# Kernel optimization log

Hardware: AMD Instinct MI355X
Metric: run time of the kernel (lower is better)

## Reference

```python
import jax, jax.numpy as jnp
import numpy as np
from jax import lax

EPS = 1e-12

def _l2norm(v, axis):
    n = jnp.linalg.norm(v, axis=axis, keepdims=True)
    return v / jnp.maximum(n, EPS)

def setup_inputs() -> dict:
    key = jax.random.key(0)
    k1, k2, k3 = jax.random.split(key, 3)
    C, H, W, K = 512, 192, 192, 64
    x = jax.random.normal(k1, (C, H, W), dtype=jnp.float32)
    conv_w = jax.random.normal(k2, (K, C), dtype=jnp.float32) * 0.05  # 1x1 conv, no bias (vladv2=False)
    centroids = jax.random.uniform(k3, (K, C), dtype=jnp.float32)
    return {"x": x, "conv_w": conv_w, "centroids": centroids}

def reference(x, conv_w, centroids):
    K = conv_w.shape[0]
    x4 = x[None]                      # [1,C,H,W]
    N, C, H, W = x4.shape
    L = H * W
    # descriptor-wise L2 normalization over channels
    x4 = _l2norm(x4, axis=1)
    # 1x1 conv -> soft assignment over clusters
    logits = jnp.einsum('kc,nchw->nkhw', conv_w, x4)
    soft = jax.nn.softmax(logits, axis=1)          # [N,K,H,W]
    sa_flat = soft.reshape(N, K, L)
    # top-2 cluster indices per location (argmax + second largest)
    _, top2 = lax.top_k(sa_flat.transpose(0, 2, 1), 2)  # [N,L,2]
    first, second = top2[..., 0], top2[..., 1]
    # unfold 3x3, padding 1: windows [N, L, K, 9] in (kh,kw) order
    pad = jnp.pad(soft, ((0, 0), (0, 0), (1, 1), (1, 1)))
    patches = jnp.stack([pad[:, :, di:di + H, dj:dj + W]
                         for di in range(3) for dj in range(3)], axis=2)  # [N,K,9,H,W]
    windows = patches.reshape(N, K, 9, L).transpose(0, 3, 1, 2)           # [N,L,K,9]
    # keep only windows of the top-2 clusters at each location
    karange = jnp.arange(K)[None, None, :]
    keep = (karange == first[:, :, None]) | (karange == second[:, :, None])  # [N,L,K]
    wsel = windows * keep[..., None].astype(windows.dtype)
    # fold (transpose of unfold): overlap-add back to [N,K,H,W]
    ws = wsel.transpose(0, 2, 3, 1).reshape(N, K, 9, H, W)
    out_pad = jnp.zeros((N, K, H + 2, W + 2), dtype=ws.dtype)
    t = 0
    for di in range(3):
        for dj in range(3):
            out_pad = out_pad.at[:, :, di:di + H, dj:dj + W].add(ws[:, :, t])
            t += 1
    weight = out_pad[:, :, 1:H + 1, 1:W + 1]
    # border mask: (min distance to border)^4
    ii = jnp.arange(H); jj = jnp.arange(W)
    mi = jnp.minimum(H - 1 - ii, ii)[:, None]
    mj = jnp.minimum(W - 1 - jj, jj)[None, :]
    m = jnp.minimum(mi, mj).astype(weight.dtype)
    m2 = m * m
    mask = m2 * m2
    weight = weight * mask[None, None]
    sa2 = weight.reshape(N, K, L)
    # per-cluster residual accumulation, vectorized (replaces the 64-iter loop)
    xf = x4.reshape(N, C, L)
    vlad = jnp.einsum('nkl,ncl->nkc', sa2, xf) - sa2.sum(-1)[..., None] * centroids[None]
    vlad = _l2norm(vlad, axis=2)               # intra-normalization
    v = vlad.reshape(N, -1)
    v = _l2norm(v, axis=1)
    return v
```

## Files before the change

kernel.cpp:

```cpp
#include <hip/hip_runtime.h>

#define HH 192
#define WW 192
#define LL (HH * WW)
#define CC 512
#define KK 64
#define EPSF 1e-12f
typedef unsigned long long ull;
typedef unsigned int uint;
typedef unsigned short ushort;

#define NCHUNK 192
#define CHUNKL (LL / NCHUNK)

typedef short bf16x8 __attribute__((ext_vector_type(8)));
typedef float f32x4 __attribute__((ext_vector_type(4)));

__device__ inline void split3(float v, ushort& h, ushort& md, ushort& lo) {
    uint b  = __float_as_uint(v);
    uint hb = b & 0xFFFF0000u;
    float r1 = v - __uint_as_float(hb);
    uint mb = __float_as_uint(r1) & 0xFFFF0000u;
    float r2 = r1 - __uint_as_float(mb);
    uint lb = __float_as_uint(r2) & 0xFFFF0000u;
    h = (ushort)(hb >> 16); md = (ushort)(mb >> 16); lo = (ushort)(lb >> 16);
}

__device__ inline void split2(float v, ushort& h, ushort& lo) {
    uint b  = __float_as_uint(v);
    uint hb = b & 0xFFFF0000u;
    float r = v - __uint_as_float(hb);
    h = (ushort)(hb >> 16); lo = (ushort)(__float_as_uint(r) >> 16);
}

__global__ __launch_bounds__(256) void k0_prep(const float* __restrict__ w,
                                               ushort* __restrict__ Whi,
                                               ushort* __restrict__ Wmid,
                                               ushort* __restrict__ Wlo,
                                               float* __restrict__ Szero) {
    int idx = blockIdx.x * 256 + threadIdx.x;
    int k = idx >> 9;
    int c = idx & 511;
    int s = c >> 5, w32 = c & 31, quad = w32 >> 3, j = w32 & 7;
    int kg = k >> 4, m = k & 15;
    int dst = (((s * 4 + kg) * 4 + quad) * 16 + m) * 8 + j;
    float v = w[idx];
    ushort h, md, lo;
    split3(v, h, md, lo);
    Whi[dst] = h; Wmid[dst] = md; Wlo[dst] = lo;
    if (blockIdx.x == 0 && threadIdx.x < 128) Szero[threadIdx.x] = 0.f;
}

__global__ __launch_bounds__(256) void k1_logits(const float* __restrict__ x,
                                                 const ushort* __restrict__ Whi,
                                                 const ushort* __restrict__ Wmid,
                                                 const ushort* __restrict__ Wlo,
                                                 float* __restrict__ soft,
                                                 float* __restrict__ invn,
                                                 ull* __restrict__ keep) {
    __shared__ float accL[3][32][64];
    __shared__ float ssL[3][2][64];
    int t = threadIdx.x, lane = t & 63, wid = t >> 6;
    int m = lane & 15, quad = lane >> 4;
    int pb = blockIdx.x * 32;
    int s16base = wid * 4;

    f32x4 acc[4][2];
#pragma unroll
    for (int kg = 0; kg < 4; ++kg)
#pragma unroll
        for (int cg = 0; cg < 2; ++cg) acc[kg][cg] = (f32x4){0.f, 0.f, 0.f, 0.f};
    float ssA[2] = {0.f, 0.f};

    const float* xq = x + (size_t)(wid * 128 + quad * 8) * LL + pb + m;

    bf16x8 Ah[2][4], Am[2][4], Al[2][4];
    float xv[2][2][8];

#pragma unroll
    for (int kg = 0; kg < 4; ++kg) {
        size_t off = (size_t)(((s16base * 4 + kg) * 64 + lane) * 8);
        Ah[0][kg] = *(const bf16x8*)(Whi  + off);
        Am[0][kg] = *(const bf16x8*)(Wmid + off);
        Al[0][kg] = *(const bf16x8*)(Wlo  + off);
    }
#pragma unroll
    for (int j = 0; j < 8; ++j) {
        const float* xr = xq + (size_t)j * LL;
        xv[0][0][j] = xr[0];
        xv[0][1][j] = xr[16];
    }

#pragma unroll
    for (int s = 0; s < 4; ++s) {
        const int cur = s & 1, nxt = cur ^ 1;
        if (s < 3) {
            int s16 = s16base + s + 1;
#pragma unroll
            for (int kg = 0; kg < 4; ++kg) {
                size_t off = (size_t)(((s16 * 4 + kg) * 64 + lane) * 8);
                Ah[nxt][kg] = *(const bf16x8*)(Whi  + off);
                Am[nxt][kg] = *(const bf16x8*)(Wmid + off);
                Al[nxt][kg] = *(const bf16x8*)(Wlo  + off);
            }
            const float* xp = xq + (size_t)(s + 1) * 32 * LL;
#pragma unroll
            for (int j = 0; j < 8; ++j) {
                const float* xr = xp + (size_t)j * LL;
                xv[nxt][0][j] = xr[0];
                xv[nxt][1][j] = xr[16];
            }
        }
        __builtin_amdgcn_sched_barrier(0);

        bf16x8 Bh[2], Bm[2], Bl[2];
#pragma unroll
        for (int cg = 0; cg < 2; ++cg)
#pragma unroll
            for (int j = 0; j < 8; ++j) {
                float v = xv[cur][cg][j];
                ssA[cg] = fmaf(v, v, ssA[cg]);
                ushort h, md, lo;
                split3(v, h, md, lo);
                Bh[cg][j] = (short)h; Bm[cg][j] = (short)md; Bl[cg][j] = (short)lo;
            }
#pragma unroll
        for (int kg = 0; kg < 4; ++kg)
#pragma unroll
            for (int cg = 0; cg < 2; ++cg) {
                f32x4 a = acc[kg][cg];
                a = __builtin_amdgcn_mfma_f32_16x16x32_bf16(Ah[cur][kg], Bh[cg], a, 0, 0, 0);
                a = __builtin_amdgcn_mfma_f32_16x16x32_bf16(Ah[cur][kg], Bm[cg], a, 0, 0, 0);
                a = __builtin_amdgcn_mfma_f32_16x16x32_bf16(Am[cur][kg], Bh[cg], a, 0, 0, 0);
                a = __builtin_amdgcn_mfma_f32_16x16x32_bf16(Ah[cur][kg], Bl[cg], a, 0, 0, 0);
                a = __builtin_amdgcn_mfma_f32_16x16x32_bf16(Al[cur][kg], Bh[cg], a, 0, 0, 0);
                a = __builtin_amdgcn_mfma_f32_16x16x32_bf16(Am[cur][kg], Bm[cg], a, 0, 0, 0);
                acc[kg][cg] = a;
            }
    }

    if (wid != 0) {
#pragma unroll
        for (int kg = 0; kg < 4; ++kg)
#pragma unroll
            for (int cg = 0; cg < 2; ++cg)
#pragma unroll
                for (int r = 0; r < 4; ++r)
                    accL[wid - 1][kg * 8 + cg * 4 + r][lane] = acc[kg][cg][r];
        ssL[wid - 1][0][lane] = ssA[0];
        ssL[wid - 1][1][lane] = ssA[1];
    }
    __syncthreads();
    if (wid != 0) return;
#pragma unroll
    for (int q = 0; q < 3; ++q) {
#pragma unroll
        for (int kg = 0; kg < 4; ++kg)
#pragma unroll
            for (int cg = 0; cg < 2; ++cg)
#pragma unroll
                for (int r = 0; r < 4; ++r)
                    acc[kg][cg][r] += accL[q][kg * 8 + cg * 4 + r][lane];
        ssA[0] += ssL[q][0][lane];
        ssA[1] += ssL[q][1][lane];
    }

#pragma unroll
    for (int cg = 0; cg < 2; ++cg) {
        float ssv = ssA[cg];
        ssv += __shfl_xor(ssv, 16);
        ssv += __shfl_xor(ssv, 32);
        float iv = 1.0f / fmaxf(sqrtf(ssv), EPSF);
        int px = pb + cg * 16 + m;
        if (quad == 0) invn[px] = iv;

        float lg[16];
        float M1 = -3.0e38f, M2 = -3.0e38f; int I1 = 0, I2 = 0;
#pragma unroll
        for (int kg = 0; kg < 4; ++kg)
#pragma unroll
            for (int r = 0; r < 4; ++r) {
                float v = acc[kg][cg][r] * iv;
                lg[kg * 4 + r] = v;
                int kk = kg * 16 + quad * 4 + r;
                if (v > M1)      { M2 = M1; I2 = I1; M1 = v; I1 = kk; }
                else if (v > M2) { M2 = v; I2 = kk; }
            }
#pragma unroll
        for (int st = 0; st < 2; ++st) {
            int d = 16 << st;
            float a1 = __shfl_xor(M1, d); int b1 = __shfl_xor(I1, d);
            float a2 = __shfl_xor(M2, d); int b2 = __shfl_xor(I2, d);
            if (a1 > M1 || (a1 == M1 && b1 < I1)) { M2 = M1; I2 = I1; M1 = a1; I1 = b1; }
            else if (a1 > M2 || (a1 == M2 && b1 < I2)) { M2 = a1; I2 = b1; }
            if (a2 > M1 || (a2 == M1 && b2 < I1)) { M2 = M1; I2 = I1; M1 = a2; I1 = b2; }
            else if (a2 > M2 || (a2 == M2 && b2 < I2)) { M2 = a2; I2 = b2; }
        }

        float es = 0.f;
#pragma unroll
        for (int q = 0; q < 16; ++q) { float e = __expf(lg[q] - M1); lg[q] = e; es += e; }
        es += __shfl_xor(es, 16);
        es += __shfl_xor(es, 32);
        float rs = 1.0f / es;

        float4* sp = (float4*)(soft + (size_t)px * KK + quad * 4);
#pragma unroll
        for (int kg = 0; kg < 4; ++kg) {
            float4 o;
            o.x = lg[kg * 4 + 0] * rs; o.y = lg[kg * 4 + 1] * rs;
            o.z = lg[kg * 4 + 2] * rs; o.w = lg[kg * 4 + 3] * rs;
            sp[kg * 4] = o;
        }
        if (quad == 0) keep[px] = (1ull << I1) | (1ull << I2);
    }
}

__global__ __launch_bounds__(256) void k2_weight(const float* __restrict__ soft,
                                                 const ull* __restrict__ keep,
                                                 const float* __restrict__ invn,
                                                 float* __restrict__ S,
                                                 ushort* __restrict__ w2t_hi,
                                                 ushort* __restrict__ w2t_lo) {
    __shared__ float sred[4][64];
    int t = threadIdx.x, lane = t & 63, wid = t >> 6;
    int l0 = blockIdx.x * 32 + wid * 8;
    float sk = 0.f;
    bf16x8 hv, lv;
#pragma unroll
    for (int p = 0; p < 8; ++p) {
        int l = l0 + p;
        int i = l / WW, j = l % WW;
        int m = min(min(i, HH - 1 - i), min(j, WW - 1 - j));
        float bm = (float)m; bm *= bm; bm *= bm;
        int cnt = 0;
#pragma unroll
        for (int di = -1; di <= 1; ++di) {
            int ii = i + di;
            if (ii < 0 || ii >= HH) continue;
#pragma unroll
            for (int dj = -1; dj <= 1; ++dj) {
                int jj = j + dj;
                if (jj < 0 || jj >= WW) continue;
                ull nb = keep[ii * WW + jj];
                cnt += (int)((nb >> lane) & 1ull);
            }
        }
        float v = soft[(size_t)l * KK + lane];
        float u = v * (float)cnt * bm;
        sk += u;
        float w2v = u * invn[l];
        ushort h, lo;
        split2(w2v, h, lo);
        hv[p] = (short)h; lv[p] = (short)lo;
    }
    size_t off = (size_t)((((l0 >> 5) * 4 + (lane >> 4)) * 64 + ((l0 >> 3) & 3) * 16 + (lane & 15)) * 8);
    *(bf16x8*)(w2t_hi + off) = hv;
    *(bf16x8*)(w2t_lo + off) = lv;
    sred[wid][lane] = sk;
    __syncthreads();
    if (wid == 0)
        atomicAdd(&S[lane], sred[0][lane] + sred[1][lane] + sred[2][lane] + sred[3][lane]);
}

__global__ __launch_bounds__(256) void k3_mfma(const ushort* __restrict__ w2t_hi,
                                               const ushort* __restrict__ w2t_lo,
                                               const float* __restrict__ x,
                                               float* __restrict__ partials) {
    int chunk = blockIdx.x;
    int c0 = blockIdx.y * 128;
    int l0 = chunk * CHUNKL;
    int t = threadIdx.x, lane = t & 63, wid = t >> 6;
    int m = lane & 15, quad = lane >> 4;

    f32x4 acc[4][2];
#pragma unroll
    for (int kg = 0; kg < 4; ++kg)
#pragma unroll
        for (int cg = 0; cg < 2; ++cg) acc[kg][cg] = (f32x4){0.f, 0.f, 0.f, 0.f};

    const float* xb = x + (size_t)(c0 + wid * 32 + m) * LL + l0 + quad * 8;

#pragma unroll
    for (int lb = 0; lb < CHUNKL; lb += 32) {
        int lstep = (l0 + lb) >> 5;
        bf16x8 Ah[4], Al[4];
#pragma unroll
        for (int kg = 0; kg < 4; ++kg) {
            size_t off = (size_t)(((lstep * 4 + kg) * 64 + lane) * 8);
            Ah[kg] = *(const bf16x8*)(w2t_hi + off);
            Al[kg] = *(const bf16x8*)(w2t_lo + off);
        }
        bf16x8 Bh[2], Bl[2];
#pragma unroll
        for (int cg = 0; cg < 2; ++cg) {
            const float* xr = xb + (size_t)(cg * 16) * LL + lb;
            float4 v0 = *(const float4*)xr;
            float4 v1 = *(const float4*)(xr + 4);
            float vv[8] = {v0.x, v0.y, v0.z, v0.w, v1.x, v1.y, v1.z, v1.w};
#pragma unroll
            for (int j = 0; j < 8; ++j) {
                ushort h, lo;
                split2(vv[j], h, lo);
                Bh[cg][j] = (short)h; Bl[cg][j] = (short)lo;
            }
        }
#pragma unroll
        for (int cg = 0; cg < 2; ++cg)
#pragma unroll
            for (int kg = 0; kg < 4; ++kg) {
                acc[kg][cg] = __builtin_amdgcn_mfma_f32_16x16x32_bf16(Ah[kg], Bh[cg], acc[kg][cg], 0, 0, 0);
                acc[kg][cg] = __builtin_amdgcn_mfma_f32_16x16x32_bf16(Ah[kg], Bl[cg], acc[kg][cg], 0, 0, 0);
                acc[kg][cg] = __builtin_amdgcn_mfma_f32_16x16x32_bf16(Al[kg], Bh[cg], acc[kg][cg], 0, 0, 0);
            }
    }
    float* pp = partials + (size_t)chunk * KK * CC;
#pragma unroll
    for (int kg = 0; kg < 4; ++kg)
#pragma unroll
        for (int cg = 0; cg < 2; ++cg) {
            int cout = c0 + wid * 32 + cg * 16 + m;
#pragma unroll
            for (int r = 0; r < 4; ++r) {
                int kout = kg * 16 + quad * 4 + r;
                pp[(size_t)kout * CC + cout] = acc[kg][cg][r];
            }
        }
}

__global__ __launch_bounds__(512) void k4a_reduce(const float* __restrict__ partials,
                                                  const float* __restrict__ S,
                                                  const float* __restrict__ cent,
                                                  float* __restrict__ vlad,
                                                  float* __restrict__ rowsq) {
    __shared__ float red[512];
    int k = blockIdx.x;
    int ci = threadIdx.x & 127;
    int c = blockIdx.y * 128 + ci;
    int q = threadIdx.x >> 7;
    const float* pk = partials + (size_t)q * (NCHUNK / 4) * KK * CC + (size_t)k * CC + c;
    float s0 = 0.f, s1 = 0.f, s2 = 0.f, s3 = 0.f;
    for (int ch = 0; ch < NCHUNK / 4; ch += 4) {
        s0 += pk[(size_t)(ch + 0) * KK * CC];
        s1 += pk[(size_t)(ch + 1) * KK * CC];
        s2 += pk[(size_t)(ch + 2) * KK * CC];
        s3 += pk[(size_t)(ch + 3) * KK * CC];
    }
    red[threadIdx.x] = (s0 + s1) + (s2 + s3);
    __syncthreads();
    float vsq = 0.f;
    if (q == 0) {
        float v = red[ci] + red[ci + 128] + red[ci + 256] + red[ci + 384];
        v -= S[k] * cent[k * CC + c];
        vlad[k * CC + c] = v;
        vsq = v * v;
    }
    __syncthreads();
    red[threadIdx.x] = vsq;
    __syncthreads();
    for (int off = 256; off > 0; off >>= 1) {
        if (threadIdx.x < off) red[threadIdx.x] += red[threadIdx.x + off];
        __syncthreads();
    }
    if (threadIdx.x == 0) atomicAdd(&rowsq[k], red[0]);
}

__global__ __launch_bounds__(256) void k4c_finish(const float* __restrict__ vlad,
                                                  const float* __restrict__ rowsq,
                                                  float* __restrict__ out) {
    __shared__ float rns[64];
    int t = threadIdx.x;
    if (t < 64) {
        float tot = rowsq[t];
        float r = 1.0f / fmaxf(sqrtf(tot), EPSF);
        float contrib = tot * r * r;
#pragma unroll
        for (int off = 32; off; off >>= 1) contrib += __shfl_xor(contrib, off, 64);
        float ginv = 1.0f / fmaxf(sqrtf(contrib), EPSF);
        rns[t] = r * ginv;
    }
    __syncthreads();
    int idx4 = blockIdx.x * 256 + t;
    int k = idx4 >> 7;
    float s = rns[k];
    float4 v = ((const float4*)vlad)[idx4];
    v.x *= s; v.y *= s; v.z *= s; v.w *= s;
    ((float4*)out)[idx4] = v;
}

extern "C" void kernel_launch(void* const* d_in, const int* in_sizes, int n_in,
                              void* d_out, int out_size, void* d_ws, size_t ws_size,
                              hipStream_t stream) {
    const float* x      = (const float*)d_in[0];
    const float* conv_w = (const float*)d_in[1];
    const float* cent   = (const float*)d_in[2];
    float* out = (float*)d_out;

    float* ws    = (float*)d_ws;
    ushort* Whi  = (ushort*)ws;
    ushort* Wmid = Whi + 32768;
    ushort* Wlo  = Wmid + 32768;
    float* soft  = ws + 49152;
    float* invn  = soft + (size_t)KK * LL;
    float* S     = invn + LL;
    float* rowsq = S + KK;
    float* vlad  = rowsq + KK;
    ull*   keep  = (ull*)(vlad + 32768);
    ushort* w2t_hi = (ushort*)(keep + LL);
    ushort* w2t_lo = w2t_hi + (size_t)LL * KK;
    float* partials = (float*)(w2t_lo + (size_t)LL * KK);

    k0_prep<<<(KK * CC) / 256, 256, 0, stream>>>(conv_w, Whi, Wmid, Wlo, S);
    k1_logits<<<LL / 32, 256, 0, stream>>>(x, Whi, Wmid, Wlo, soft, invn, keep);
    k2_weight<<<LL / 32, 256, 0, stream>>>(soft, keep, invn, S, w2t_hi, w2t_lo);
    k3_mfma<<<dim3(NCHUNK, 4), 256, 0, stream>>>(w2t_hi, w2t_lo, x, partials);
    k4a_reduce<<<dim3(KK, 4), 512, 0, stream>>>(partials, S, cent, vlad, rowsq);
    k4c_finish<<<(KK * CC / 4) / 256, 256, 0, stream>>>(vlad, rowsq, out);
}
```

Measured before the change: 198.3 us.

## Restructure logits kernel: per-wave pixel split with LDS-staged x via global_load_lds

The logits kernel previously split the channel dimension across four waves, each covering 32 pixels, and reduced the partial accumulators through shared memory. Now each block covers 64 pixels and each wave owns 16 of them across all 512 channels, so the cross-wave reduction is gone. x tiles are double-buffered in LDS using direct global-to-LDS 16-byte loads, which gives wider coalesced reads. The cost is a block-wide barrier on every one of the 16 channel steps, and the weight fragments are now loaded inside the loop without prefetch, which may expose load latency.

```diff
diff --git a/kernel.cpp b/kernel.cpp
--- a/kernel.cpp
+++ b/kernel.cpp
@@ -15,6 +15,11 @@
 
 typedef short bf16x8 __attribute__((ext_vector_type(8)));
 typedef float f32x4 __attribute__((ext_vector_type(4)));
+
+__device__ __forceinline__ void gl16(const float* g, float* l) {
+    __builtin_amdgcn_global_load_lds((const __attribute__((address_space(1))) void*)g,
+                                     (__attribute__((address_space(3))) void*)l, 16, 0, 0);
+}
 
 __device__ inline void split3(float v, ushort& h, ushort& md, ushort& lo) {
     uint b  = __float_as_uint(v);
@@ -58,162 +63,109 @@
                                                  float* __restrict__ soft,
                                                  float* __restrict__ invn,
                                                  ull* __restrict__ keep) {
-    __shared__ float accL[3][32][64];
-    __shared__ float ssL[3][2][64];
+    __shared__ float xs[2][32][64];
     int t = threadIdx.x, lane = t & 63, wid = t >> 6;
     int m = lane & 15, quad = lane >> 4;
-    int pb = blockIdx.x * 32;
-    int s16base = wid * 4;
-
-    f32x4 acc[4][2];
+    int pb = blockIdx.x * 64;
+
+    f32x4 acc[4];
+#pragma unroll
+    for (int kg = 0; kg < 4; ++kg) acc[kg] = (f32x4){0.f, 0.f, 0.f, 0.f};
+    float ss = 0.f;
+
+    const float* gbase = x + (size_t)(4 * wid + quad) * LL + pb + m * 4;
+
+    gl16(gbase, &xs[0][4 * wid][0]);
+    gl16(gbase + (size_t)16 * LL, &xs[0][16 + 4 * wid][0]);
+
+    int cur = 0;
+#pragma unroll
+    for (int s = 0; s < 16; ++s) {
+        __syncthreads();
+        if (s < 15) {
+            const float* g = gbase + (size_t)(s + 1) * 32 * LL;
+            gl16(g, &xs[cur ^ 1][4 * wid][0]);
+            gl16(g + (size_t)16 * LL, &xs[cur ^ 1][16 + 4 * wid][0]);
+        }
+        bf16x8 Ah[4], Am[4], Al[4];
+#pragma unroll
+        for (int kg = 0; kg < 4; ++kg) {
+            size_t off = (size_t)(((s * 4 + kg) * 64 + lane) * 8);
+            Ah[kg] = *(const bf16x8*)(Whi  + off);
+            Am[kg] = *(const bf16x8*)(Wmid + off);
+            Al[kg] = *(const bf16x8*)(Wlo  + off);
+        }
+        float xv[8];
+#pragma unroll
+        for (int j = 0; j < 8; ++j) xv[j] = xs[cur][quad * 8 + j][wid * 16 + m];
+        bf16x8 Bh, Bm, Bl;
+#pragma unroll
+        for (int j = 0; j < 8; ++j) {
+            float v = xv[j];
+            ss = fmaf(v, v, ss);
+            ushort h, md, lo;
+            split3(v, h, md, lo);
+            Bh[j] = (short)h; Bm[j] = (short)md; Bl[j] = (short)lo;
+        }
+#pragma unroll
+        for (int kg = 0; kg < 4; ++kg) {
+            f32x4 a = acc[kg];
+            a = __builtin_amdgcn_mfma_f32_16x16x32_bf16(Ah[kg], Bh, a, 0, 0, 0);
+            a = __builtin_amdgcn_mfma_f32_16x16x32_bf16(Ah[kg], Bm, a, 0, 0, 0);
+            a = __builtin_amdgcn_mfma_f32_16x16x32_bf16(Am[kg], Bh, a, 0, 0, 0);
+            a = __builtin_amdgcn_mfma_f32_16x16x32_bf16(Ah[kg], Bl, a, 0, 0, 0);
+            a = __builtin_amdgcn_mfma_f32_16x16x32_bf16(Al[kg], Bh, a, 0, 0, 0);
+            a = __builtin_amdgcn_mfma_f32_16x16x32_bf16(Am[kg], Bm, a, 0, 0, 0);
+            acc[kg] = a;
+        }
+        cur ^= 1;
+    }
+
+    ss += __shfl_xor(ss, 16);
+    ss += __shfl_xor(ss, 32);
+    float iv = 1.0f / fmaxf(sqrtf(ss), EPSF);
+    int px = pb + wid * 16 + m;
+    if (quad == 0) invn[px] = iv;
+
+    float lg[16];
+    float M1 = -3.0e38f, M2 = -3.0e38f; int I1 = 0, I2 = 0;
 #pragma unroll
     for (int kg = 0; kg < 4; ++kg)
 #pragma unroll
-        for (int cg = 0; cg < 2; ++cg) acc[kg][cg] = (f32x4){0.f, 0.f, 0.f, 0.f};
-    float ssA[2] = {0.f, 0.f};
-
-    const float* xq = x + (size_t)(wid * 128 + quad * 8) * LL + pb + m;
-
-    bf16x8 Ah[2][4], Am[2][4], Al[2][4];
-    float xv[2][2][8];
-
+        for (int r = 0; r < 4; ++r) {
+            float v = acc[kg][r] * iv;
+            lg[kg * 4 + r] = v;
+            int kk = kg * 16 + quad * 4 + r;
+            if (v > M1)      { M2 = M1; I2 = I1; M1 = v; I1 = kk; }
+            else if (v > M2) { M2 = v; I2 = kk; }
+        }
+#pragma unroll
+    for (int st = 0; st < 2; ++st) {
+        int d = 16 << st;
+        float a1 = __shfl_xor(M1, d); int b1 = __shfl_xor(I1, d);
+        float a2 = __shfl_xor(M2, d); int b2 = __shfl_xor(I2, d);
+        if (a1 > M1 || (a1 == M1 && b1 < I1)) { M2 = M1; I2 = I1; M1 = a1; I1 = b1; }
+        else if (a1 > M2 || (a1 == M2 && b1 < I2)) { M2 = a1; I2 = b1; }
+        if (a2 > M1 || (a2 == M1 && b2 < I1)) { M2 = M1; I2 = I1; M1 = a2; I1 = b2; }
+        else if (a2 > M2 || (a2 == M2 && b2 < I2)) { M2 = a2; I2 = b2; }
+    }
+
+    float es = 0.f;
+#pragma unroll
+    for (int q = 0; q < 16; ++q) { float e = __expf(lg[q] - M1); lg[q] = e; es += e; }
+    es += __shfl_xor(es, 16);
+    es += __shfl_xor(es, 32);
+    float rs = 1.0f / es;
+
+    float4* sp = (float4*)(soft + (size_t)px * KK + quad * 4);
 #pragma unroll
     for (int kg = 0; kg < 4; ++kg) {
-        size_t off = (size_t)(((s16base * 4 + kg) * 64 + lane) * 8);
-        Ah[0][kg] = *(const bf16x8*)(Whi  + off);
-        Am[0][kg] = *(const bf16x8*)(Wmid + off);
-        Al[0][kg] = *(const bf16x8*)(Wlo  + off);
-    }
-#pragma unroll
-    for (int j = 0; j < 8; ++j) {
-        const float* xr = xq + (size_t)j * LL;
-        xv[0][0][j] = xr[0];
-        xv[0][1][j] = xr[16];
-    }
-
-#pragma unroll
-    for (int s = 0; s < 4; ++s) {
-        const int cur = s & 1, nxt = cur ^ 1;
-        if (s < 3) {
-            int s16 = s16base + s + 1;
-#pragma unroll
-            for (int kg = 0; kg < 4; ++kg) {
-                size_t off = (size_t)(((s16 * 4 + kg) * 64 + lane) * 8);
-                Ah[nxt][kg] = *(const bf16x8*)(Whi  + off);
-                Am[nxt][kg] = *(const bf16x8*)(Wmid + off);
-                Al[nxt][kg] = *(const bf16x8*)(Wlo  + off);
-            }
-            const float* xp = xq + (size_t)(s + 1) * 32 * LL;
-#pragma unroll
-            for (int j = 0; j < 8; ++j) {
-                const float* xr = xp + (size_t)j * LL;
-                xv[nxt][0][j] = xr[0];
-                xv[nxt][1][j] = xr[16];
-            }
-        }
-        __builtin_amdgcn_sched_barrier(0);
-
-        bf16x8 Bh[2], Bm[2], Bl[2];
-#pragma unroll
-        for (int cg = 0; cg < 2; ++cg)
-#pragma unroll
-            for (int j = 0; j < 8; ++j) {
-                float v = xv[cur][cg][j];
-                ssA[cg] = fmaf(v, v, ssA[cg]);
-                ushort h, md, lo;
-                split3(v, h, md, lo);
-                Bh[cg][j] = (short)h; Bm[cg][j] = (short)md; Bl[cg][j] = (short)lo;
-            }
-#pragma unroll
-        for (int kg = 0; kg < 4; ++kg)
-#pragma unroll
-            for (int cg = 0; cg < 2; ++cg) {
-                f32x4 a = acc[kg][cg];
-                a = __builtin_amdgcn_mfma_f32_16x16x32_bf16(Ah[cur][kg], Bh[cg], a, 0, 0, 0);
-                a = __builtin_amdgcn_mfma_f32_16x16x32_bf16(Ah[cur][kg], Bm[cg], a, 0, 0, 0);
-                a = __builtin_amdgcn_mfma_f32_16x16x32_bf16(Am[cur][kg], Bh[cg], a, 0, 0, 0);
-                a = __builtin_amdgcn_mfma_f32_16x16x32_bf16(Ah[cur][kg], Bl[cg], a, 0, 0, 0);
-                a = __builtin_amdgcn_mfma_f32_16x16x32_bf16(Al[cur][kg], Bh[cg], a, 0, 0, 0);
-                a = __builtin_amdgcn_mfma_f32_16x16x32_bf16(Am[cur][kg], Bm[cg], a, 0, 0, 0);
-                acc[kg][cg] = a;
-            }
-    }
-
-    if (wid != 0) {
-#pragma unroll
-        for (int kg = 0; kg < 4; ++kg)
-#pragma unroll
-            for (int cg = 0; cg < 2; ++cg)
-#pragma unroll
-                for (int r = 0; r < 4; ++r)
-                    accL[wid - 1][kg * 8 + cg * 4 + r][lane] = acc[kg][cg][r];
-        ssL[wid - 1][0][lane] = ssA[0];
-        ssL[wid - 1][1][lane] = ssA[1];
-    }
-    __syncthreads();
-    if (wid != 0) return;
-#pragma unroll
-    for (int q = 0; q < 3; ++q) {
-#pragma unroll
-        for (int kg = 0; kg < 4; ++kg)
-#pragma unroll
-            for (int cg = 0; cg < 2; ++cg)
-#pragma unroll
-                for (int r = 0; r < 4; ++r)
-                    acc[kg][cg][r] += accL[q][kg * 8 + cg * 4 + r][lane];
-        ssA[0] += ssL[q][0][lane];
-        ssA[1] += ssL[q][1][lane];
-    }
-
-#pragma unroll
-    for (int cg = 0; cg < 2; ++cg) {
-        float ssv = ssA[cg];
-        ssv += __shfl_xor(ssv, 16);
-        ssv += __shfl_xor(ssv, 32);
-        float iv = 1.0f / fmaxf(sqrtf(ssv), EPSF);
-        int px = pb + cg * 16 + m;
-        if (quad == 0) invn[px] = iv;
-
-        float lg[16];
-        float M1 = -3.0e38f, M2 = -3.0e38f; int I1 = 0, I2 = 0;
-#pragma unroll
-        for (int kg = 0; kg < 4; ++kg)
-#pragma unroll
-            for (int r = 0; r < 4; ++r) {
-                float v = acc[kg][cg][r] * iv;
-                lg[kg * 4 + r] = v;
-                int kk = kg * 16 + quad * 4 + r;
-                if (v > M1)      { M2 = M1; I2 = I1; M1 = v; I1 = kk; }
-                else if (v > M2) { M2 = v; I2 = kk; }
-            }
-#pragma unroll
-        for (int st = 0; st < 2; ++st) {
-            int d = 16 << st;
-            float a1 = __shfl_xor(M1, d); int b1 = __shfl_xor(I1, d);
-            float a2 = __shfl_xor(M2, d); int b2 = __shfl_xor(I2, d);
-            if (a1 > M1 || (a1 == M1 && b1 < I1)) { M2 = M1; I2 = I1; M1 = a1; I1 = b1; }
-            else if (a1 > M2 || (a1 == M2 && b1 < I2)) { M2 = a1; I2 = b1; }
-            if (a2 > M1 || (a2 == M1 && b2 < I1)) { M2 = M1; I2 = I1; M1 = a2; I1 = b2; }
-            else if (a2 > M2 || (a2 == M2 && b2 < I2)) { M2 = a2; I2 = b2; }
-        }
-
-        float es = 0.f;
-#pragma unroll
-        for (int q = 0; q < 16; ++q) { float e = __expf(lg[q] - M1); lg[q] = e; es += e; }
-        es += __shfl_xor(es, 16);
-        es += __shfl_xor(es, 32);
-        float rs = 1.0f / es;
-
-        float4* sp = (float4*)(soft + (size_t)px * KK + quad * 4);
-#pragma unroll
-        for (int kg = 0; kg < 4; ++kg) {
-            float4 o;
-            o.x = lg[kg * 4 + 0] * rs; o.y = lg[kg * 4 + 1] * rs;
-            o.z = lg[kg * 4 + 2] * rs; o.w = lg[kg * 4 + 3] * rs;
-            sp[kg * 4] = o;
-        }
-        if (quad == 0) keep[px] = (1ull << I1) | (1ull << I2);
-    }
+        float4 o;
+        o.x = lg[kg * 4 + 0] * rs; o.y = lg[kg * 4 + 1] * rs;
+        o.z = lg[kg * 4 + 2] * rs; o.w = lg[kg * 4 + 3] * rs;
+        sp[kg * 4] = o;
+    }
+    if (quad == 0) keep[px] = (1ull << I1) | (1ull << I2);
 }
 
 __global__ __launch_bounds__(256) void k2_weight(const float* __restrict__ soft,
@@ -411,7 +363,7 @@
     float* partials = (float*)(w2t_lo + (size_t)LL * KK);
 
     k0_prep<<<(KK * CC) / 256, 256, 0, stream>>>(conv_w, Whi, Wmid, Wlo, S);
-    k1_logits<<<LL / 32, 256, 0, stream>>>(x, Whi, Wmid, Wlo, soft, invn, keep);
+    k1_logits<<<LL / 64, 256, 0, stream>>>(x, Whi, Wmid, Wlo, soft, invn, keep);
     k2_weight<<<LL / 32, 256, 0, stream>>>(soft, keep, invn, S, w2t_hi, w2t_lo);
     k3_mfma<<<dim3(NCHUNK, 4), 256, 0, stream>>>(w2t_hi, w2t_lo, x, partials);
     k4a_reduce<<<dim3(KK, 4), 512, 0, stream>>>(partials, S, cent, vlad, rowsq);
```

Result: slower. 204.3 us (+3.1%).
